# Optimization experiments

Hardware: AMD Instinct MI355X
Metric: run time of the kernel (lower is better)

## Reference

```python
import jax, jax.numpy as jnp
import numpy as np

N = 100000      # nodes
E = 1600000     # edges (avg degree 16)
IN_DIM = 64
OUT_DIM = 128
BN_EPS = 1e-5


def setup_inputs() -> dict:
    key = jax.random.key(0)
    kx, ke, kw, kb, ks = jax.random.split(key, 5)
    x = jax.random.normal(kx, (N, IN_DIM), dtype=jnp.float32)
    edge_index = jax.random.randint(ke, (2, E), 0, N, dtype=jnp.int32)
    # GCNConv linear weight (no bias inside lin; conv bias separate)
    W = jax.random.normal(kw, (IN_DIM, OUT_DIM), dtype=jnp.float32) / np.sqrt(IN_DIM)
    bias = jax.random.normal(kb, (OUT_DIM,), dtype=jnp.float32) * 0.01
    # skip projection Linear(in_dim, out_dim, bias=False)
    skip_W = jax.random.normal(ks, (IN_DIM, OUT_DIM), dtype=jnp.float32) / np.sqrt(IN_DIM)
    # BatchNorm1d affine params (training-mode batch stats used in forward)
    gamma = jnp.ones((OUT_DIM,), dtype=jnp.float32)
    beta = jnp.zeros((OUT_DIM,), dtype=jnp.float32)
    return {"x": x, "edge_index": edge_index, "W": W, "bias": bias,
            "skip_W": skip_W, "gamma": gamma, "beta": beta}


def _gcn_forward(x, edge_index, W, bias, skip_W, gamma, beta):
    n = x.shape[0]
    # GCNConv, normalize=True, add_self_loops=True (PyG defaults)
    row, col = edge_index[0], edge_index[1]
    loop = jnp.arange(n, dtype=edge_index.dtype)
    row_f = jnp.concatenate([row, loop])   # source nodes
    col_f = jnp.concatenate([col, loop])   # target nodes

    xt = x @ W                             # [N, OUT]
    deg = jax.ops.segment_sum(jnp.ones_like(col_f, dtype=xt.dtype), col_f,
                              num_segments=n)          # >= 1 due to self loops
    dinv = jax.lax.rsqrt(deg)
    norm = dinv[row_f] * dinv[col_f]                    # [E+N]
    msgs = xt[row_f] * norm[:, None]                    # gather + scale
    out = jax.ops.segment_sum(msgs, col_f, num_segments=n) + bias

    # skip-sum (in_dim != out_dim -> project)
    out = out + x @ skip_W

    # BatchNorm1d (training-mode batch statistics), affine
    mean = out.mean(axis=0)
    var = out.var(axis=0)
    out = (out - mean) * jax.lax.rsqrt(var + BN_EPS) * gamma + beta

    # ReLU; dropout p=0.0 -> identity
    return jax.nn.relu(out)


def reference(x, edge_index, W, bias, skip_W, gamma, beta):
    return _gcn_forward(x, edge_index, W, bias, skip_W, gamma, beta)
```

## Files before the change

kernel.cpp:

```cpp
#include <hip/hip_runtime.h>


typedef unsigned short ushort;
typedef __bf16 bf16x8 __attribute__((ext_vector_type(8)));
typedef float f32x4 __attribute__((ext_vector_type(4)));
typedef float f32x2 __attribute__((ext_vector_type(2)));
typedef ushort u16x8 __attribute__((ext_vector_type(8)));

constexpr int N_NODES = 100000;
constexpr int N_PAD   = 100096;
constexpr int E_EDGES = 1600000;

constexpr int BUCK_SHIFT = 7;
constexpr int NBUCK   = (N_NODES + 127) / 128;
constexpr int NBUCK_P = 784;
constexpr int CHUNK   = 8192;
constexpr int NCHUNK  = (E_EDGES + CHUNK - 1) / CHUNK;
constexpr int GH_STRIDE = 200;
constexpr int SORT_CAP = 4096;
constexpr int GG      = 256;

constexpr size_t OFF_SCALE  = 0;
constexpr size_t OFF_DINV   = 256;
constexpr size_t OFF_ROWPTR = 100352;
constexpr size_t OFF_BASE   = 200480;
constexpr size_t OFF_GHIST  = 201280;
constexpr size_t OFF_BINNED = 358080;
constexpr size_t OFF_PART   = OFF_BINNED;
constexpr size_t OFF_A      = 1958080;
constexpr size_t OFF_PRE    = 8364224;
constexpr size_t OFF_XD8    = OFF_PRE;
constexpr size_t OFF_BT     = 14770368;
constexpr size_t OFF_TICK   = 14778560;

static __device__ __forceinline__ ushort f2bf(float f) {
    union { float f; unsigned u; } v; v.f = f;
    unsigned r = v.u + 0x7FFFu + ((v.u >> 16) & 1u);
    return (ushort)(r >> 16);
}
static __device__ __forceinline__ float bf2f(ushort u) {
    union { unsigned u; float f; } v; v.u = (unsigned)u << 16;
    return v.f;
}
static __device__ __forceinline__ unsigned pack_fp8x4(float a, float b, float c, float d) {
    int r = 0;
    r = __builtin_amdgcn_cvt_pk_fp8_f32(a, b, r, false);
    r = __builtin_amdgcn_cvt_pk_fp8_f32(c, d, r, true);
    return (unsigned)r;
}

__global__ __launch_bounds__(256) void k_hist(const int* __restrict__ col,
                                              int* __restrict__ gh_t,
                                              const float* __restrict__ W,
                                              const float* __restrict__ skipW,
                                              ushort* __restrict__ Bt,
                                              unsigned* __restrict__ tick) {
    int c = blockIdx.x, t = threadIdx.x;
    if (c >= NCHUNK) {
        int idx = (c - NCHUNK) * 256 + t;
        if (c == NCHUNK && t < 2) tick[t] = 0u;
        int k = idx >> 7, n = idx & 127;
        float v = (k < 64) ? W[k * 128 + n] : skipW[(k - 64) * 128 + n];
        Bt[n * 128 + k] = f2bf(v);
        return;
    }
    __shared__ int h[NBUCK_P];
    for (int b = t; b < NBUCK_P; b += 256) h[b] = 0;
    __syncthreads();
    const int4* col4 = (const int4*)col;
    int g0 = c * (CHUNK / 4);
#pragma unroll
    for (int i = 0; i < CHUNK / 1024; ++i) {
        int g4 = g0 + i * 256 + t;
        if (g4 * 4 + 3 < E_EDGES) {
            int4 cc = col4[g4];
            atomicAdd(&h[cc.x >> BUCK_SHIFT], 1);
            atomicAdd(&h[cc.y >> BUCK_SHIFT], 1);
            atomicAdd(&h[cc.z >> BUCK_SHIFT], 1);
            atomicAdd(&h[cc.w >> BUCK_SHIFT], 1);
        } else {
#pragma unroll
            for (int j = 0; j < 4; ++j) {
                int e = g4 * 4 + j;
                if (e < E_EDGES) atomicAdd(&h[col[e] >> BUCK_SHIFT], 1);
            }
        }
    }
    __syncthreads();
    for (int b = t; b < NBUCK_P; b += 256) gh_t[(size_t)b * GH_STRIDE + c] = h[b];
}

__global__ __launch_bounds__(256) void k_scan(int* __restrict__ gh_t,
                                              int* __restrict__ base,
                                              int* __restrict__ rowptr,
                                              unsigned* __restrict__ tick) {
    __shared__ int wtot[4];
    __shared__ int amlast;
    int w = threadIdx.x >> 6, l = threadIdx.x & 63;
    int b = blockIdx.x * 4 + w;
    int* rowp = gh_t + (size_t)b * GH_STRIDE;
    int carry = 0;
#pragma unroll
    for (int i = 0; i < 4; ++i) {
        int idx = i * 64 + l;
        int v = (idx < NCHUNK) ? rowp[idx] : 0;
        int orig = v;
#pragma unroll
        for (int d = 1; d < 64; d <<= 1) {
            int o = __shfl_up(v, d);
            if (l >= d) v += o;
        }
        if (idx < NCHUNK) rowp[idx] = carry + v - orig;
        carry += __shfl(v, 63);
    }
    if (l == 0 && b < NBUCK) atomicExch(&base[b], carry);
    __syncthreads();
    if (threadIdx.x == 0)
        amlast = (atomicAdd(tick + 0, 1u) == (unsigned)(gridDim.x - 1)) ? 1 : 0;
    __syncthreads();
    if (!amlast) return;

    int t = threadIdx.x;
    int i0 = t * 4;
    int v0 = (i0 + 0 < NBUCK) ? atomicAdd(&base[i0 + 0], 0) : 0;
    int v1 = (i0 + 1 < NBUCK) ? atomicAdd(&base[i0 + 1], 0) : 0;
    int v2 = (i0 + 2 < NBUCK) ? atomicAdd(&base[i0 + 2], 0) : 0;
    int v3 = (i0 + 3 < NBUCK) ? atomicAdd(&base[i0 + 3], 0) : 0;
    int s = v0 + v1 + v2 + v3;
    int incl = s;
#pragma unroll
    for (int d = 1; d < 64; d <<= 1) {
        int o = __shfl_up(incl, d);
        if (l >= d) incl += o;
    }
    if (l == 63) wtot[w] = incl;
    __syncthreads();
    int wpre = 0;
    for (int ww = 0; ww < w; ++ww) wpre += wtot[ww];
    int excl = wpre + incl - s;
    if (i0 + 0 < NBUCK) base[i0 + 0] = excl;
    if (i0 + 1 < NBUCK) base[i0 + 1] = excl + v0;
    if (i0 + 2 < NBUCK) base[i0 + 2] = excl + v0 + v1;
    if (i0 + 3 < NBUCK) base[i0 + 3] = excl + v0 + v1 + v2;
    if (t == 255) {
        int total = wpre + incl;
        base[NBUCK] = total;
        rowptr[N_NODES] = total;
    }
}

__global__ __launch_bounds__(256) void k_scatter_bin(const int* __restrict__ row,
                                                     const int* __restrict__ col,
                                                     const int* __restrict__ gh_t,
                                                     const int* __restrict__ base,
                                                     unsigned int* __restrict__ binned) {
    __shared__ int cur[NBUCK_P];
    int c = blockIdx.x, t = threadIdx.x;
    for (int b = t; b < NBUCK_P; b += 256) {
        int bb = (b < NBUCK) ? base[b] : 0;
        cur[b] = bb + gh_t[(size_t)b * GH_STRIDE + c];
    }
    __syncthreads();
    const int4* col4 = (const int4*)col;
    const int4* row4 = (const int4*)row;
    int g0 = c * (CHUNK / 4);
#pragma unroll
    for (int i = 0; i < CHUNK / 1024; ++i) {
        int g4 = g0 + i * 256 + t;
        if (g4 * 4 + 3 < E_EDGES) {
            int4 cc = col4[g4];
            int4 rr = row4[g4];
            int p;
            p = atomicAdd(&cur[cc.x >> BUCK_SHIFT], 1);
            binned[p] = ((unsigned)(cc.x & 127) << 17) | (unsigned)rr.x;
            p = atomicAdd(&cur[cc.y >> BUCK_SHIFT], 1);
            binned[p] = ((unsigned)(cc.y & 127) << 17) | (unsigned)rr.y;
            p = atomicAdd(&cur[cc.z >> BUCK_SHIFT], 1);
            binned[p] = ((unsigned)(cc.z & 127) << 17) | (unsigned)rr.z;
            p = atomicAdd(&cur[cc.w >> BUCK_SHIFT], 1);
            binned[p] = ((unsigned)(cc.w & 127) << 17) | (unsigned)rr.w;
        } else {
#pragma unroll
            for (int j = 0; j < 4; ++j) {
                int e = g4 * 4 + j;
                if (e < E_EDGES) {
                    int d = col[e], s = row[e];
                    int p = atomicAdd(&cur[d >> BUCK_SHIFT], 1);
                    binned[p] = ((unsigned)(d & 127) << 17) | (unsigned)s;
                }
            }
        }
    }
}

__global__ __launch_bounds__(256) void k_sortbucket(unsigned int* __restrict__ binned,
                                                    const int* __restrict__ base,
                                                    int* __restrict__ rowptr,
                                                    float* __restrict__ dinv,
                                                    const float* __restrict__ x,
                                                    unsigned* __restrict__ xd8,
                                                    ushort* __restrict__ A) {
    __shared__ unsigned int ebuf[SORT_CAP];
    __shared__ int sbuf[SORT_CAP];
    __shared__ int lcnt[128];
    __shared__ int lptr[128];
    __shared__ float ldinv[128];
    __shared__ int wsum[2];
    int b = blockIdx.x, t = threadIdx.x;
    int i0 = base[b], i1 = base[b + 1];
    int cnt = i1 - i0;
    if (cnt > SORT_CAP) cnt = SORT_CAP;
    int n0 = b << BUCK_SHIFT;
    int nn = min(128, N_NODES - n0);

    for (int k = t; k < cnt; k += 256) ebuf[k] = binned[i0 + k];
    if (t < 128) lcnt[t] = 0;
    __syncthreads();
    for (int k = t; k < cnt; k += 256) atomicAdd(&lcnt[ebuf[k] >> 17], 1);
    __syncthreads();

    int myc = 0, val = 0;
    if (t < 128) {
        myc = lcnt[t];
        val = myc;
#pragma unroll
        for (int d = 1; d < 64; d <<= 1) {
            int o = __shfl_up(val, d);
            if ((t & 63) >= d) val += o;
        }
        if ((t & 63) == 63) wsum[t >> 6] = val;
    }
    __syncthreads();
    if (t < 128) {
        if (t >= 64) val += wsum[0];
        int excl = val - myc;
        lptr[t] = excl;
        float dv = rsqrtf((float)myc + 1.0f);
        ldinv[t] = dv;
        if (t < nn) {
            rowptr[n0 + t] = i0 + excl;
            dinv[n0 + t] = dv;
        }
    }
    __syncthreads();
    for (int k = t; k < cnt; k += 256) {
        unsigned int e = ebuf[k];
        int j = (int)(e >> 17);
        int p = atomicAdd(&lptr[j], 1);
        sbuf[p] = (int)(e & 0x1FFFF);
    }
    __syncthreads();
    for (int k = t; k < cnt; k += 256) binned[i0 + k] = (unsigned int)sbuf[k];

#pragma unroll
    for (int it = 0; it < 8; ++it) {
        int idx = it * 256 + t;
        int nl = idx >> 4, q = idx & 15;
        int c = n0 + nl;
        unsigned w8 = 0;
        ushort4 xb = {0, 0, 0, 0};
        if (nl < nn) {
            float4 v = ((const float4*)x)[(size_t)c * 16 + q];
            float d = ldinv[nl];
            w8 = pack_fp8x4(v.x * d, v.y * d, v.z * d, v.w * d);
            xb.x = f2bf(v.x); xb.y = f2bf(v.y); xb.z = f2bf(v.z); xb.w = f2bf(v.w);
        }
        xd8[(size_t)c * 16 + q] = w8;
        ((ushort4*)A)[(size_t)c * 32 + 16 + q] = xb;
    }
}

__global__ __launch_bounds__(256) void k_agg(const unsigned* __restrict__ xd8,
                                             const float* __restrict__ dinv,
                                             const int* __restrict__ rowptr,
                                             const unsigned int* __restrict__ csr,
                                             ushort* __restrict__ A) {
    int t = blockIdx.x * blockDim.x + threadIdx.x;
    if (t >= N_PAD * 16) return;
    int c = t >> 4;
    int q = t & 15;
    if (c >= N_NODES) {
        ushort4 z = {0, 0, 0, 0};
        ((ushort4*)A)[(size_t)c * 32 + q] = z;
        return;
    }
    float dc = dinv[c];
    float4 acc;
    {
        unsigned w = xd8[t];
        f32x2 lo = __builtin_amdgcn_cvt_pk_f32_fp8((int)w, false);
        f32x2 hi = __builtin_amdgcn_cvt_pk_f32_fp8((int)w, true);
        acc.x = lo.x; acc.y = lo.y; acc.z = hi.x; acc.w = hi.y;
    }
    int i0 = rowptr[c], i1 = rowptr[c + 1];
    int i = i0;
    for (; i + 8 <= i1; i += 8) {
        int s[8];
#pragma unroll
        for (int k = 0; k < 8; ++k) s[k] = (int)csr[i + k];
        unsigned w[8];
#pragma unroll
        for (int k = 0; k < 8; ++k) w[k] = xd8[s[k] * 16 + q];
#pragma unroll
        for (int k = 0; k < 8; ++k) {
            f32x2 lo = __builtin_amdgcn_cvt_pk_f32_fp8((int)w[k], false);
            f32x2 hi = __builtin_amdgcn_cvt_pk_f32_fp8((int)w[k], true);
            acc.x += lo.x; acc.y += lo.y; acc.z += hi.x; acc.w += hi.y;
        }
    }
    for (; i < i1; ++i) {
        unsigned w = xd8[(int)csr[i] * 16 + q];
        f32x2 lo = __builtin_amdgcn_cvt_pk_f32_fp8((int)w, false);
        f32x2 hi = __builtin_amdgcn_cvt_pk_f32_fp8((int)w, true);
        acc.x += lo.x; acc.y += lo.y; acc.z += hi.x; acc.w += hi.y;
    }
    ushort4 o;
    o.x = f2bf(acc.x * dc); o.y = f2bf(acc.y * dc);
    o.z = f2bf(acc.z * dc); o.w = f2bf(acc.w * dc);
    ((ushort4*)A)[(size_t)c * 32 + q] = o;
}

__global__ __launch_bounds__(512, 2) void k_gemm(const ushort* __restrict__ A,
                                                 const ushort* __restrict__ Bt,
                                                 ushort* __restrict__ pre,
                                                 float* __restrict__ partial) {
    __shared__ float sred[128];
    __shared__ float qred[128];
    int tid = threadIdx.x;
    int wave = tid >> 6, lane = tid & 63;
    int wm = wave >> 2, wn = wave & 3;
    int l15 = lane & 15, quad = lane >> 4;
    int col0 = wn * 32;

    if (tid < 128) { sred[tid] = 0.f; qred[tid] = 0.f; }
    __syncthreads();

    bf16x8 bf_[4][2];
#pragma unroll
    for (int kc = 0; kc < 4; ++kc)
#pragma unroll
        for (int jc = 0; jc < 2; ++jc)
            bf_[kc][jc] = *(const bf16x8*)&Bt[(size_t)(col0 + jc * 16 + l15) * 128 + kc * 32 + quad * 8];

    float lsum[8] = {0.f, 0.f, 0.f, 0.f, 0.f, 0.f, 0.f, 0.f};
    float lsq[8]  = {0.f, 0.f, 0.f, 0.f, 0.f, 0.f, 0.f, 0.f};

    for (int ci = blockIdx.x; ci < NBUCK; ci += GG) {
        int row0 = ci * 128 + wm * 64;
        bf16x8 af[4][4];
#pragma unroll
        for (int kc = 0; kc < 4; ++kc)
#pragma unroll
            for (int ir = 0; ir < 4; ++ir)
                af[kc][ir] = *(const bf16x8*)&A[(size_t)(row0 + ir * 16 + l15) * 128 + kc * 32 + quad * 8];

        f32x4 acc[4][2];
#pragma unroll
        for (int ir = 0; ir < 4; ++ir)
#pragma unroll
            for (int jc = 0; jc < 2; ++jc) acc[ir][jc] = (f32x4){0.f, 0.f, 0.f, 0.f};

#pragma unroll
        for (int kc = 0; kc < 4; ++kc)
#pragma unroll
            for (int ir = 0; ir < 4; ++ir)
#pragma unroll
                for (int jc = 0; jc < 2; ++jc)
                    acc[ir][jc] = __builtin_amdgcn_mfma_f32_16x16x32_bf16(
                        bf_[kc][jc], af[kc][ir], acc[ir][jc], 0, 0, 0);

#pragma unroll
        for (int ir = 0; ir < 4; ++ir) {
            int row = row0 + ir * 16 + l15;
            bool live = row < N_NODES;
#pragma unroll
            for (int jc = 0; jc < 2; ++jc) {
                ushort4 o;
                o.x = f2bf(acc[ir][jc][0]); o.y = f2bf(acc[ir][jc][1]);
                o.z = f2bf(acc[ir][jc][2]); o.w = f2bf(acc[ir][jc][3]);
                *(ushort4*)&pre[(size_t)row * 128 + col0 + jc * 16 + quad * 4] = o;
                if (live) {
#pragma unroll
                    for (int r = 0; r < 4; ++r) {
                        float v = acc[ir][jc][r];
                        lsum[jc * 4 + r] += v;
                        lsq[jc * 4 + r]  += v * v;
                    }
                }
            }
        }
    }

#pragma unroll
    for (int m = 1; m < 16; m <<= 1) {
#pragma unroll
        for (int i = 0; i < 8; ++i) {
            lsum[i] += __shfl_xor(lsum[i], m);
            lsq[i]  += __shfl_xor(lsq[i], m);
        }
    }
    if (l15 == 0) {
#pragma unroll
        for (int jc = 0; jc < 2; ++jc)
#pragma unroll
            for (int r = 0; r < 4; ++r) {
                int c = col0 + jc * 16 + quad * 4 + r;
                atomicAdd(&sred[c], lsum[jc * 4 + r]);
                atomicAdd(&qred[c], lsq[jc * 4 + r]);
            }
    }
    __syncthreads();
    if (tid < 128) {
        partial[(size_t)blockIdx.x * 256 + tid]       = sred[tid];
        partial[(size_t)blockIdx.x * 256 + 128 + tid] = qred[tid];
    }
}

__global__ __launch_bounds__(256) void k_reduce(const float* __restrict__ partial,
                                                const float* __restrict__ gamma,
                                                const float* __restrict__ beta,
                                                float* __restrict__ scaleshift) {
    __shared__ float ls[256], lq[256];
    int j = blockIdx.x;
    int t = threadIdx.x;
    float s = 0.f, q = 0.f;
    for (int p = t; p < GG; p += 256) {
        s += partial[(size_t)p * 256 + j];
        q += partial[(size_t)p * 256 + 128 + j];
    }
    ls[t] = s; lq[t] = q;
    __syncthreads();
#pragma unroll
    for (int off = 128; off > 0; off >>= 1) {
        if (t < off) { ls[t] += ls[t + off]; lq[t] += lq[t + off]; }
        __syncthreads();
    }
    if (t == 0) {
        float mean = ls[0] * (1.0f / N_NODES);
        float var  = lq[0] * (1.0f / N_NODES) - mean * mean;
        float sc   = gamma[j] * rsqrtf(var + 1e-5f);
        scaleshift[j]       = sc;
        scaleshift[128 + j] = beta[j] - mean * sc;
    }
}

__global__ __launch_bounds__(256) void k_apply(const ushort* __restrict__ pre,
                                               float* __restrict__ out,
                                               const float* __restrict__ ss) {
    int t = blockIdx.x * blockDim.x + threadIdx.x;
    if (t >= N_NODES * 16) return;
    int j8 = t & 15;
    u16x8 p = ((const u16x8*)pre)[t];
    float4 sc0 = ((const float4*)ss)[j8 * 2];
    float4 sc1 = ((const float4*)ss)[j8 * 2 + 1];
    float4 sh0 = ((const float4*)(ss + 128))[j8 * 2];
    float4 sh1 = ((const float4*)(ss + 128))[j8 * 2 + 1];
    float4 v0, v1;
    v0.x = fmaxf(fmaf(bf2f(p[0]), sc0.x, sh0.x), 0.f);
    v0.y = fmaxf(fmaf(bf2f(p[1]), sc0.y, sh0.y), 0.f);
    v0.z = fmaxf(fmaf(bf2f(p[2]), sc0.z, sh0.z), 0.f);
    v0.w = fmaxf(fmaf(bf2f(p[3]), sc0.w, sh0.w), 0.f);
    v1.x = fmaxf(fmaf(bf2f(p[4]), sc1.x, sh1.x), 0.f);
    v1.y = fmaxf(fmaf(bf2f(p[5]), sc1.y, sh1.y), 0.f);
    v1.z = fmaxf(fmaf(bf2f(p[6]), sc1.z, sh1.z), 0.f);
    v1.w = fmaxf(fmaf(bf2f(p[7]), sc1.w, sh1.w), 0.f);
    ((float4*)out)[t * 2]     = v0;
    ((float4*)out)[t * 2 + 1] = v1;
}

extern "C" void kernel_launch(void* const* d_in, const int* in_sizes, int n_in,
                              void* d_out, int out_size, void* d_ws, size_t ws_size,
                              hipStream_t stream) {
    const float* x      = (const float*)d_in[0];
    const int*   eidx   = (const int*)d_in[1];
    const float* W      = (const float*)d_in[2];
    const float* gamma  = (const float*)d_in[5];
    const float* beta   = (const float*)d_in[6];
    const float* skipW  = (const float*)d_in[4];
    float* out = (float*)d_out;
    float* ws  = (float*)d_ws;

    const int* row = eidx;
    const int* col = eidx + E_EDGES;

    float* scaleshift = ws + OFF_SCALE;
    float* dinv       = ws + OFF_DINV;
    int*   rowptr     = (int*)(ws + OFF_ROWPTR);
    int*   base       = (int*)(ws + OFF_BASE);
    int*   gh_t       = (int*)(ws + OFF_GHIST);
    unsigned int* binned = (unsigned int*)(ws + OFF_BINNED);
    float* partial    = ws + OFF_PART;
    ushort* A         = (ushort*)(ws + OFF_A);
    unsigned* xd8     = (unsigned*)(ws + OFF_XD8);
    ushort* pre       = (ushort*)(ws + OFF_PRE);
    ushort* Bt        = (ushort*)(ws + OFF_BT);
    unsigned* tick    = (unsigned*)(ws + OFF_TICK);

    k_hist<<<NCHUNK + 64, 256, 0, stream>>>(col, gh_t, W, skipW, Bt, tick);
    k_scan<<<NBUCK_P / 4, 256, 0, stream>>>(gh_t, base, rowptr, tick);
    k_scatter_bin<<<NCHUNK, 256, 0, stream>>>(row, col, gh_t, base, binned);
    k_sortbucket<<<NBUCK, 256, 0, stream>>>(binned, base, rowptr, dinv, x, xd8, A);
    k_agg<<<(N_PAD * 16 + 255) / 256, 256, 0, stream>>>(xd8, dinv, rowptr, binned, A);
    k_gemm<<<GG, 512, 0, stream>>>(A, Bt, pre, partial);
    k_reduce<<<128, 256, 0, stream>>>(partial, gamma, beta, scaleshift);
    k_apply<<<(N_NODES * 16 + 255) / 256, 256, 0, stream>>>(pre, out, scaleshift);
}
```

Before: 197.2 us.

## Recompute GEMM in apply pass instead of storing bf16 pre-activation buffer

The GEMM no longer writes a bf16 intermediate. A stats-only GEMM pass computes the BatchNorm sums. A second GEMM pass recomputes the product and applies the scale/shift and ReLU directly into the fp32 output. This removes a large intermediate write and read at the cost of reading A twice and redoing the MFMA work, and it also avoids bf16 rounding of the pre-activation.

```diff
diff --git a/kernel.cpp b/kernel.cpp
--- a/kernel.cpp
+++ b/kernel.cpp
@@ -5,7 +5,6 @@
 typedef __bf16 bf16x8 __attribute__((ext_vector_type(8)));
 typedef float f32x4 __attribute__((ext_vector_type(4)));
 typedef float f32x2 __attribute__((ext_vector_type(2)));
-typedef ushort u16x8 __attribute__((ext_vector_type(8)));
 
 constexpr int N_NODES = 100000;
 constexpr int N_PAD   = 100096;
@@ -28,19 +27,14 @@
 constexpr size_t OFF_BINNED = 358080;
 constexpr size_t OFF_PART   = OFF_BINNED;
 constexpr size_t OFF_A      = 1958080;
-constexpr size_t OFF_PRE    = 8364224;
-constexpr size_t OFF_XD8    = OFF_PRE;
-constexpr size_t OFF_BT     = 14770368;
-constexpr size_t OFF_TICK   = 14778560;
+constexpr size_t OFF_XD8    = 8364224;
+constexpr size_t OFF_BT     = 9965760;
+constexpr size_t OFF_TICK   = 9973952;
 
 static __device__ __forceinline__ ushort f2bf(float f) {
     union { float f; unsigned u; } v; v.f = f;
     unsigned r = v.u + 0x7FFFu + ((v.u >> 16) & 1u);
     return (ushort)(r >> 16);
-}
-static __device__ __forceinline__ float bf2f(ushort u) {
-    union { unsigned u; float f; } v; v.u = (unsigned)u << 16;
-    return v.f;
 }
 static __device__ __forceinline__ unsigned pack_fp8x4(float a, float b, float c, float d) {
     int r = 0;
@@ -320,10 +314,9 @@
     ((ushort4*)A)[(size_t)c * 32 + q] = o;
 }
 
-__global__ __launch_bounds__(512, 2) void k_gemm(const ushort* __restrict__ A,
-                                                 const ushort* __restrict__ Bt,
-                                                 ushort* __restrict__ pre,
-                                                 float* __restrict__ partial) {
+__global__ __launch_bounds__(512, 2) void k_gemm_stats(const ushort* __restrict__ A,
+                                                       const ushort* __restrict__ Bt,
+                                                       float* __restrict__ partial) {
     __shared__ float sred[128];
     __shared__ float qred[128];
     int tid = threadIdx.x;
@@ -372,21 +365,15 @@
 #pragma unroll
         for (int ir = 0; ir < 4; ++ir) {
             int row = row0 + ir * 16 + l15;
-            bool live = row < N_NODES;
-#pragma unroll
-            for (int jc = 0; jc < 2; ++jc) {
-                ushort4 o;
-                o.x = f2bf(acc[ir][jc][0]); o.y = f2bf(acc[ir][jc][1]);
-                o.z = f2bf(acc[ir][jc][2]); o.w = f2bf(acc[ir][jc][3]);
-                *(ushort4*)&pre[(size_t)row * 128 + col0 + jc * 16 + quad * 4] = o;
-                if (live) {
+            if (row < N_NODES) {
+#pragma unroll
+                for (int jc = 0; jc < 2; ++jc)
 #pragma unroll
                     for (int r = 0; r < 4; ++r) {
                         float v = acc[ir][jc][r];
                         lsum[jc * 4 + r] += v;
                         lsq[jc * 4 + r]  += v * v;
                     }
-                }
             }
         }
     }
@@ -444,28 +431,70 @@
     }
 }
 
-__global__ __launch_bounds__(256) void k_apply(const ushort* __restrict__ pre,
-                                               float* __restrict__ out,
-                                               const float* __restrict__ ss) {
-    int t = blockIdx.x * blockDim.x + threadIdx.x;
-    if (t >= N_NODES * 16) return;
-    int j8 = t & 15;
-    u16x8 p = ((const u16x8*)pre)[t];
-    float4 sc0 = ((const float4*)ss)[j8 * 2];
-    float4 sc1 = ((const float4*)ss)[j8 * 2 + 1];
-    float4 sh0 = ((const float4*)(ss + 128))[j8 * 2];
-    float4 sh1 = ((const float4*)(ss + 128))[j8 * 2 + 1];
-    float4 v0, v1;
-    v0.x = fmaxf(fmaf(bf2f(p[0]), sc0.x, sh0.x), 0.f);
-    v0.y = fmaxf(fmaf(bf2f(p[1]), sc0.y, sh0.y), 0.f);
-    v0.z = fmaxf(fmaf(bf2f(p[2]), sc0.z, sh0.z), 0.f);
-    v0.w = fmaxf(fmaf(bf2f(p[3]), sc0.w, sh0.w), 0.f);
-    v1.x = fmaxf(fmaf(bf2f(p[4]), sc1.x, sh1.x), 0.f);
-    v1.y = fmaxf(fmaf(bf2f(p[5]), sc1.y, sh1.y), 0.f);
-    v1.z = fmaxf(fmaf(bf2f(p[6]), sc1.z, sh1.z), 0.f);
-    v1.w = fmaxf(fmaf(bf2f(p[7]), sc1.w, sh1.w), 0.f);
-    ((float4*)out)[t * 2]     = v0;
-    ((float4*)out)[t * 2 + 1] = v1;
+__global__ __launch_bounds__(512, 2) void k_gemm_apply(const ushort* __restrict__ A,
+                                                       const ushort* __restrict__ Bt,
+                                                       const float* __restrict__ ss,
+                                                       float* __restrict__ out) {
+    int tid = threadIdx.x;
+    int wave = tid >> 6, lane = tid & 63;
+    int wm = wave >> 2, wn = wave & 3;
+    int l15 = lane & 15, quad = lane >> 4;
+    int col0 = wn * 32;
+
+    bf16x8 bf_[4][2];
+#pragma unroll
+    for (int kc = 0; kc < 4; ++kc)
+#pragma unroll
+        for (int jc = 0; jc < 2; ++jc)
+            bf_[kc][jc] = *(const bf16x8*)&Bt[(size_t)(col0 + jc * 16 + l15) * 128 + kc * 32 + quad * 8];
+
+    float4 sc4[2], sh4[2];
+#pragma unroll
+    for (int jc = 0; jc < 2; ++jc) {
+        sc4[jc] = *(const float4*)&ss[col0 + jc * 16 + quad * 4];
+        sh4[jc] = *(const float4*)&ss[128 + col0 + jc * 16 + quad * 4];
+    }
+
+    for (int ci = blockIdx.x; ci < NBUCK; ci += GG) {
+        int row0 = ci * 128 + wm * 64;
+        bf16x8 af[4][4];
+#pragma unroll
+        for (int kc = 0; kc < 4; ++kc)
+#pragma unroll
+            for (int ir = 0; ir < 4; ++ir)
+                af[kc][ir] = *(const bf16x8*)&A[(size_t)(row0 + ir * 16 + l15) * 128 + kc * 32 + quad * 8];
+
+        f32x4 acc[4][2];
+#pragma unroll
+        for (int ir = 0; ir < 4; ++ir)
+#pragma unroll
+            for (int jc = 0; jc < 2; ++jc) acc[ir][jc] = (f32x4){0.f, 0.f, 0.f, 0.f};
+
+#pragma unroll
+        for (int kc = 0; kc < 4; ++kc)
+#pragma unroll
+            for (int ir = 0; ir < 4; ++ir)
+#pragma unroll
+                for (int jc = 0; jc < 2; ++jc)
+                    acc[ir][jc] = __builtin_amdgcn_mfma_f32_16x16x32_bf16(
+                        bf_[kc][jc], af[kc][ir], acc[ir][jc], 0, 0, 0);
+
+#pragma unroll
+        for (int ir = 0; ir < 4; ++ir) {
+            int row = row0 + ir * 16 + l15;
+            if (row < N_NODES) {
+#pragma unroll
+                for (int jc = 0; jc < 2; ++jc) {
+                    float4 v;
+                    v.x = fmaxf(fmaf(acc[ir][jc][0], sc4[jc].x, sh4[jc].x), 0.f);
+                    v.y = fmaxf(fmaf(acc[ir][jc][1], sc4[jc].y, sh4[jc].y), 0.f);
+                    v.z = fmaxf(fmaf(acc[ir][jc][2], sc4[jc].z, sh4[jc].z), 0.f);
+                    v.w = fmaxf(fmaf(acc[ir][jc][3], sc4[jc].w, sh4[jc].w), 0.f);
+                    *(float4*)&out[(size_t)row * 128 + col0 + jc * 16 + quad * 4] = v;
+                }
+            }
+        }
+    }
 }
 
 extern "C" void kernel_launch(void* const* d_in, const int* in_sizes, int n_in,
@@ -474,9 +503,9 @@
     const float* x      = (const float*)d_in[0];
     const int*   eidx   = (const int*)d_in[1];
     const float* W      = (const float*)d_in[2];
+    const float* skipW  = (const float*)d_in[4];
     const float* gamma  = (const float*)d_in[5];
     const float* beta   = (const float*)d_in[6];
-    const float* skipW  = (const float*)d_in[4];
     float* out = (float*)d_out;
     float* ws  = (float*)d_ws;
 
@@ -492,7 +521,6 @@
     float* partial    = ws + OFF_PART;
     ushort* A         = (ushort*)(ws + OFF_A);
     unsigned* xd8     = (unsigned*)(ws + OFF_XD8);
-    ushort* pre       = (ushort*)(ws + OFF_PRE);
     ushort* Bt        = (ushort*)(ws + OFF_BT);
     unsigned* tick    = (unsigned*)(ws + OFF_TICK);
 
@@ -501,7 +529,7 @@
     k_scatter_bin<<<NCHUNK, 256, 0, stream>>>(row, col, gh_t, base, binned);
     k_sortbucket<<<NBUCK, 256, 0, stream>>>(binned, base, rowptr, dinv, x, xd8, A);
     k_agg<<<(N_PAD * 16 + 255) / 256, 256, 0, stream>>>(xd8, dinv, rowptr, binned, A);
-    k_gemm<<<GG, 512, 0, stream>>>(A, Bt, pre, partial);
+    k_gemm_stats<<<GG, 512, 0, stream>>>(A, Bt, partial);
     k_reduce<<<128, 256, 0, stream>>>(partial, gamma, beta, scaleshift);
-    k_apply<<<(N_NODES * 16 + 255) / 256, 256, 0, stream>>>(pre, out, scaleshift);
-}
+    k_gemm_apply<<<GG, 512, 0, stream>>>(A, Bt, scaleshift, out);
+}
```

After: 203.8 us. 3.3% more time.
